# Optimization experiments

Measured on AMD Instinct MI355X. Metric: run time of the kernel, lower is better.

The kernel has to match this reference:

```python
import jax, jax.numpy as jnp
import numpy as np

# ---- static config (from init_kwargs / search_cfg) ----
N, C, CI, H, W_ = 4, 64, 16, 96, 96   # frames, in_ch, inter_ch, height, width
PS, S0, WS, K = 7, 4, 9, 32           # patch size, query stride, search window, top-k
SCALE = 10.0                          # softmax_scale
WH, PP = WS // 2, PS // 2
PAD = WH + PP                         # reflect pad so every candidate patch is valid
nH = H // S0
NQ = nH * nH                          # queries per frame
D = CI * PS * PS                      # patch feature dim


def conv1x1(x, w, b):
    # x: [N,Cin,H,W], w: [Cout,Cin]
    return jnp.einsum('oc,nchw->nohw', w, x) + b[None, :, None, None]


def extract_patches(x):
    # x: [N,CI,H,W] -> [N,Ho,Wo,CI*PS*PS]; patch at index y has center y-WH in image coords
    xp = jnp.pad(x, ((0, 0), (0, 0), (PAD, PAD), (PAD, PAD)), mode='reflect')
    p = jax.lax.conv_general_dilated_patches(xp, (PS, PS), (1, 1), 'VALID')
    return jnp.transpose(p, (0, 2, 3, 1))


def setup_inputs() -> dict:
    key = jax.random.key(0)
    ks = jax.random.split(key, 6)
    s = 0.05
    return {
        'vid': jax.random.normal(ks[0], (N, C, H, W_), jnp.float32),
        'flows': jnp.zeros((N, 2, H, W_), jnp.int32),
        'theta_w': jax.random.normal(ks[1], (CI, C), jnp.float32) * s,
        'theta_b': jnp.zeros((CI,), jnp.float32),
        'phi_w': jax.random.normal(ks[2], (CI, C), jnp.float32) * s,
        'phi_b': jnp.zeros((CI,), jnp.float32),
        'g_w': jax.random.normal(ks[3], (CI, C), jnp.float32) * s,
        'g_b': jnp.zeros((CI,), jnp.float32),
        'w_w': jax.random.normal(ks[4], (C, CI), jnp.float32) * s,
        'w_b': jnp.zeros((C,), jnp.float32),
    }


def reference(vid, flows, theta_w, theta_b, phi_w, phi_b, g_w, g_b, w_w, w_b):
    theta = conv1x1(vid, theta_w, theta_b)   # queries
    phi = conv1x1(vid, phi_w, phi_b)         # keys
    g = conv1x1(vid, g_w, g_b)               # values

    Tp = extract_patches(theta)  # [N,Ho,Wo,D]
    Pp = extract_patches(phi)
    Gp = extract_patches(g)

    # query grid centers (stride0)
    q = jnp.arange(0, H, S0)
    qci = jnp.repeat(q, nH)      # [NQ]
    qcj = jnp.tile(q, nH)

    # flow-guided candidate window (stride1=1, ws x ws offsets)
    off = jnp.arange(WS) - WH
    oi = jnp.repeat(off, WS)     # [WS*WS]
    oj = jnp.tile(off, WS)
    fq = flows[:, :, qci, qcj]   # [N,2,NQ] integer flow at query centers
    ci = jnp.clip(qci[None, :, None] + fq[:, 0, :, None] + oi[None, None, :], 0, H - 1)
    cj = jnp.clip(qcj[None, :, None] + fq[:, 1, :, None] + oj[None, None, :], 0, W_ - 1)
    Yi, Yj = ci + WH, cj + WH    # [N,NQ,WS*WS] indices into patch arrays

    gather = jax.vmap(lambda P, yi, yj: P[yi, yj])

    Qp = Tp[:, qci + WH, qcj + WH, :]            # [N,NQ,D]
    Cg = gather(Pp, Yi, Yj)                      # [N,NQ,WS*WS,D]
    # L2 patch distances
    dist = ((Qp ** 2).sum(-1)[:, :, None] + (Cg ** 2).sum(-1)
            - 2.0 * jnp.einsum('nqd,nqwd->nqw', Qp, Cg))

    negd, idx = jax.lax.top_k(-dist, K)          # k nearest patches
    w = jax.nn.softmax(SCALE * negd, axis=-1)    # softmax(-scale * dist)

    yi_k = jnp.take_along_axis(Yi, idx, axis=2)  # [N,NQ,K]
    yj_k = jnp.take_along_axis(Yj, idx, axis=2)
    Gg = gather(Gp, yi_k, yj_k)                  # [N,NQ,K,D]

    # wpsum: weighted patch sum
    outp = jnp.einsum('nqk,nqkd->nqd', w, Gg).reshape(N, NQ, CI, PS, PS)
    vals = jnp.transpose(outp, (0, 1, 3, 4, 2))  # [N,NQ,PS,PS,CI]

    # fold (overlap-add) back to image, normalized by counts
    ii2 = (qci[:, None] + jnp.arange(PS))[:, :, None]   # [NQ,PS,1] canvas rows
    jj2 = (qcj[:, None] + jnp.arange(PS))[:, None, :]   # [NQ,1,PS] canvas cols
    Hc, Wc = H + 2 * PP, W_ + 2 * PP
    canvas = jnp.zeros((N, Hc, Wc, CI), vid.dtype).at[:, ii2, jj2, :].add(vals)
    cnt = jnp.zeros((Hc, Wc), vid.dtype).at[ii2, jj2].add(jnp.ones((NQ, PS, PS), vid.dtype))
    agg = canvas[:, PP:PP + H, PP:PP + W_] / cnt[PP:PP + H, PP:PP + W_, None]
    agg = jnp.transpose(agg, (0, 3, 1, 2))       # [N,CI,H,W]

    return vid + conv1x1(agg, w_w, w_b)
```

## Files before the change

### kernel.cpp

```cpp
#include <hip/hip_runtime.h>
#include <hip/hip_bf16.h>

#define N_   4
#define C_   64
#define CI_  16
#define H_   96
#define W__  96
#define PS_  7
#define S0_  4
#define WS_  9
#define K_   32
#define WH_  4
#define PP_  3
#define nH_  24
#define NQ_  576
#define D_   784
#define HW_  9216

#define PLS  226
#define QLS  52

__device__ __forceinline__ int rf(int v) {
    v = v < 0 ? -v : v;
    return v > H_ - 1 ? 2 * (H_ - 1) - v : v;
}

__global__ __launch_bounds__(256) void conv_kernel(
    const float* __restrict__ vid,
    const float* __restrict__ tw, const float* __restrict__ tb,
    const float* __restrict__ pw, const float* __restrict__ pb,
    const float* __restrict__ gw, const float* __restrict__ gb,
    float* __restrict__ theta, float* __restrict__ phi, float* __restrict__ g)
{
    int b = blockIdx.x;
    int pbk = b % 144;
    int t2  = b / 144;
    int og  = t2 & 1;
    int arr = t2 >> 1;
    const float* wsel = arr == 0 ? tw : (arr == 1 ? pw : gw);
    const float* bsel = arr == 0 ? tb : (arr == 1 ? pb : gb);
    float*       dsel = arr == 0 ? theta : (arr == 1 ? phi : g);

    int idx = pbk * 256 + threadIdx.x;
    int n = idx / HW_, pix = idx % HW_;
    const float* vp = vid + (size_t)n * C_ * HW_ + pix;
    const float* wp = wsel + og * 8 * C_;

    float acc[8];
#pragma unroll
    for (int o = 0; o < 8; o++) acc[o] = 0.f;

#pragma unroll
    for (int cc = 0; cc < C_; cc += 8) {
        float v[8];
#pragma unroll
        for (int j = 0; j < 8; j++) v[j] = vp[(cc + j) * HW_];
#pragma unroll
        for (int o = 0; o < 8; o++) {
            float4 wa = *(const float4*)&wp[o * C_ + cc];
            float4 wbv = *(const float4*)&wp[o * C_ + cc + 4];
            acc[o] += wa.x * v[0] + wa.y * v[1] + wa.z * v[2] + wa.w * v[3]
                    + wbv.x * v[4] + wbv.y * v[5] + wbv.z * v[6] + wbv.w * v[7];
        }
    }

    size_t ob = (size_t)idx * CI_ + og * 8;
    *(float4*)&dsel[ob + 0] = make_float4(acc[0] + bsel[og * 8 + 0],
                                          acc[1] + bsel[og * 8 + 1],
                                          acc[2] + bsel[og * 8 + 2],
                                          acc[3] + bsel[og * 8 + 3]);
    *(float4*)&dsel[ob + 4] = make_float4(acc[4] + bsel[og * 8 + 4],
                                          acc[5] + bsel[og * 8 + 5],
                                          acc[6] + bsel[og * 8 + 6],
                                          acc[7] + bsel[og * 8 + 7]);
}

__global__ __launch_bounds__(192) void attn_kernel(
    const float* __restrict__ theta, const float* __restrict__ phi,
    const float* __restrict__ g, const int* __restrict__ flows,
    float* __restrict__ outp)
{
    __shared__ float Ql[CI_ * QLS];
    __shared__ float Pl[CI_ * PLS];
    __shared__ float Gl[CI_ * PLS];
    __shared__ float part[81 * 17];
    __shared__ float dist[81];
    __shared__ int   selflag[81];
    __shared__ float wlist[K_];
    __shared__ int   cilist[K_], cjlist[K_];
    __shared__ float dmin_s, esum_s;

    int tid = threadIdx.x;
    int bq  = blockIdx.x;
    int n = bq / NQ_, q0 = bq % NQ_;
    int qi = q0 / nH_, qj = q0 % nH_;
    int qci = qi * S0_, qcj = qj * S0_;

    int f0 = flows[((n * 2 + 0) * H_ + qci) * W__ + qcj];
    int f1 = flows[((n * 2 + 1) * H_ + qci) * W__ + qcj];
    int bi = qci + f0, bj = qcj + f1;
    int loi = min(max(bi - WH_, 0), H_ - 1);
    int loj = min(max(bj - WH_, 0), W__ - 1);

    const float* thn = theta + (size_t)n * HW_ * CI_;
    const float* phn = phi   + (size_t)n * HW_ * CI_;
    const float* gn  = g     + (size_t)n * HW_ * CI_;

    for (int i = tid; i < 49 * 4; i += 192) {
        int px = i >> 2, cg = (i & 3) * 4;
        int r = px / 7, s = px % 7;
        size_t gb = ((size_t)(rf(qci + r - PP_) * W__ + rf(qcj + s - PP_))) * CI_ + cg;
        float4 v = *(const float4*)&thn[gb];
        Ql[(cg + 0) * QLS + px] = v.x;
        Ql[(cg + 1) * QLS + px] = v.y;
        Ql[(cg + 2) * QLS + px] = v.z;
        Ql[(cg + 3) * QLS + px] = v.w;
    }
    for (int i = tid; i < 225 * 4; i += 192) {
        int px = i >> 2, cg = (i & 3) * 4;
        int r = px / 15, s = px % 15;
        size_t gb = ((size_t)(rf(loi + r - PP_) * W__ + rf(loj + s - PP_))) * CI_ + cg;
        float4 pv = *(const float4*)&phn[gb];
        float4 gv = *(const float4*)&gn[gb];
        Pl[(cg + 0) * PLS + px] = pv.x;
        Pl[(cg + 1) * PLS + px] = pv.y;
        Pl[(cg + 2) * PLS + px] = pv.z;
        Pl[(cg + 3) * PLS + px] = pv.w;
        Gl[(cg + 0) * PLS + px] = gv.x;
        Gl[(cg + 1) * PLS + px] = gv.y;
        Gl[(cg + 2) * PLS + px] = gv.z;
        Gl[(cg + 3) * PLS + px] = gv.w;
    }
    if (tid == 0) esum_s = 0.f;
    __syncthreads();

    if (tid < 144) {
        int c  = tid & 15;
        int cj = tid >> 4;
        float qr[49];
#pragma unroll
        for (int i = 0; i < 12; i++) {
            float4 t4 = *(const float4*)&Ql[c * QLS + i * 4];
            qr[i * 4 + 0] = t4.x; qr[i * 4 + 1] = t4.y;
            qr[i * 4 + 2] = t4.z; qr[i * 4 + 3] = t4.w;
        }
        qr[48] = Ql[c * QLS + 48];

        float corr[9], sqv[9];
#pragma unroll
        for (int i = 0; i < 9; i++) { corr[i] = 0.f; sqv[i] = 0.f; }

        const float* Pb = &Pl[c * PLS + cj];
#pragma unroll
        for (int y = 0; y < 15; y++) {
            float seg[7];
#pragma unroll
            for (int s = 0; s < 7; s++) seg[s] = Pb[y * 15 + s];
            float s2 = 0.f;
#pragma unroll
            for (int s = 0; s < 7; s++) s2 += seg[s] * seg[s];
#pragma unroll
            for (int ci = 0; ci < 9; ci++) {
                if (y - ci >= 0 && y - ci < 7) {
                    const int r = y - ci;
                    float t = 0.f;
#pragma unroll
                    for (int s = 0; s < 7; s++) t += qr[r * 7 + s] * seg[s];
                    corr[ci] += t;
                    sqv[ci]  += s2;
                }
            }
        }
#pragma unroll
        for (int ci = 0; ci < 9; ci++)
            part[(cj * 9 + ci) * 17 + c] = sqv[ci] - 2.f * corr[ci];
    }
    __syncthreads();

    if (tid < 81) {
        int wi = tid / WS_, wj = tid % WS_;
        int cil = min(max(bi + wi - WH_, 0), H_ - 1) - loi;
        int cjl = min(max(bj + wj - WH_, 0), W__ - 1) - loj;
        int pidx = cjl * 9 + cil;
        float d = 0.f;
#pragma unroll
        for (int c = 0; c < CI_; c++) d += part[pidx * 17 + c];
        dist[tid] = d;
    }
    __syncthreads();

    if (tid < 81) {
        float d = dist[tid];
        int rank = 0;
        for (int j = 0; j < 81; j++) {
            float dj = dist[j];
            rank += (dj < d) || (dj == d && j < tid);
        }
        selflag[tid] = (rank < K_) ? 1 : 0;
        if (rank == 0) dmin_s = d;
    }
    __syncthreads();

    float e = 0.f;
    int pos = -1;
    if (tid < 81 && selflag[tid]) {
        pos = 0;
        for (int j = 0; j < tid; j++) pos += selflag[j];
        e = expf(10.f * (dmin_s - dist[tid]));
        atomicAdd(&esum_s, e);
    }
    __syncthreads();
    if (pos >= 0) {
        int wi = tid / WS_, wj = tid % WS_;
        wlist[pos]  = e / esum_s;
        cilist[pos] = min(max(bi + wi - WH_, 0), H_ - 1) - loi;
        cjlist[pos] = min(max(bj + wj - WH_, 0), W__ - 1) - loj;
    }
    __syncthreads();

    float wreg[K_];
    int   oreg[K_];
#pragma unroll
    for (int k = 0; k < K_; k++) {
        wreg[k] = wlist[k];
        oreg[k] = cilist[k] * 15 + cjlist[k];
    }
    float* op = outp + (size_t)bq * D_;
    for (int dI = tid; dI < D_; dI += 192) {
        int rs = dI >> 4, c = dI & 15;
        int r = rs / 7, s = rs % 7;
        const float* Gb = &Gl[c * PLS + r * 15 + s];
        float acc = 0.f;
#pragma unroll
        for (int k = 0; k < K_; k++) acc += wreg[k] * Gb[oreg[k]];
        op[dI] = acc;
    }
}

__global__ __launch_bounds__(256) void output_kernel(
    const float* __restrict__ vid, const float* __restrict__ outp,
    const float* __restrict__ ww, const float* __restrict__ wb,
    float* __restrict__ out)
{
    __shared__ float part[32][4][CI_];
    __shared__ float agg_l[32][17];
    __shared__ float w_l[C_ * CI_];
    __shared__ float b_l[C_];

    int tid = threadIdx.x;
    *(float4*)&w_l[tid * 4] = *(const float4*)&ww[tid * 4];
    if (tid < C_) b_l[tid] = wb[tid];

    int gp0 = blockIdx.x * 32;

    if (tid < 128) {
        int px = tid >> 2, cb = tid & 3;
        int idx = gp0 + px;
        int n = idx / HW_, pix = idx % HW_;
        int y = pix / W__, x = pix % W__;
        int thi_i = min(nH_ - 1, (y + PP_) >> 2);
        int thi_j = min(nH_ - 1, (x + PP_) >> 2);
        int qi = (y >> 2) + (cb >> 1);
        int qj = (x >> 2) + (cb & 1);
        float4 r0 = make_float4(0.f, 0.f, 0.f, 0.f), r1 = r0, r2 = r0, r3 = r0;
        if (qi <= thi_i && qj <= thi_j) {
            int a  = y + PP_ - S0_ * qi;
            int bb = x + PP_ - S0_ * qj;
            const float* op = outp +
                (((size_t)n * NQ_ + qi * nH_ + qj) * 49 + a * 7 + bb) * CI_;
            r0 = *(const float4*)&op[0];
            r1 = *(const float4*)&op[4];
            r2 = *(const float4*)&op[8];
            r3 = *(const float4*)&op[12];
        }
        *(float4*)&part[px][cb][0]  = r0;
        *(float4*)&part[px][cb][4]  = r1;
        *(float4*)&part[px][cb][8]  = r2;
        *(float4*)&part[px][cb][12] = r3;
    }
    __syncthreads();

    {
        int px = tid >> 3, c2 = (tid & 7) * 2;
        int idx = gp0 + px;
        int pix = idx % HW_;
        int y = pix / W__, x = pix % W__;
        int ni = min(nH_ - 1, (y + PP_) >> 2) - (y >> 2) + 1;
        int nj = min(nH_ - 1, (x + PP_) >> 2) - (x >> 2) + 1;
        float inv = 1.f / (float)(ni * nj);
#pragma unroll
        for (int k = 0; k < 2; k++) {
            int c = c2 + k;
            agg_l[px][c] = (part[px][0][c] + part[px][1][c] +
                            part[px][2][c] + part[px][3][c]) * inv;
        }
    }
    __syncthreads();

    int og = tid >> 5, px = tid & 31;
    int idx = gp0 + px;
    int n = idx / HW_, pix = idx % HW_;
    float ar[CI_];
#pragma unroll
    for (int c = 0; c < CI_; c++) ar[c] = agg_l[px][c];

    const float* vp  = vid + (size_t)n * C_ * HW_ + pix;
    float*       op2 = out + (size_t)n * C_ * HW_ + pix;
#pragma unroll
    for (int o = 0; o < 8; o++) {
        int co = og * 8 + o;
        float4 w0 = *(const float4*)&w_l[co * CI_ + 0];
        float4 w1 = *(const float4*)&w_l[co * CI_ + 4];
        float4 w2 = *(const float4*)&w_l[co * CI_ + 8];
        float4 w3 = *(const float4*)&w_l[co * CI_ + 12];
        float s = b_l[co];
        s += w0.x * ar[0]  + w0.y * ar[1]  + w0.z * ar[2]  + w0.w * ar[3];
        s += w1.x * ar[4]  + w1.y * ar[5]  + w1.z * ar[6]  + w1.w * ar[7];
        s += w2.x * ar[8]  + w2.y * ar[9]  + w2.z * ar[10] + w2.w * ar[11];
        s += w3.x * ar[12] + w3.y * ar[13] + w3.z * ar[14] + w3.w * ar[15];
        op2[(size_t)co * HW_] = vp[(size_t)co * HW_] + s;
    }
}

extern "C" void kernel_launch(void* const* d_in, const int* in_sizes, int n_in,
                              void* d_out, int out_size, void* d_ws, size_t ws_size,
                              hipStream_t stream) {
    const float* vid   = (const float*)d_in[0];
    const int*   flows = (const int*)  d_in[1];
    const float* tw    = (const float*)d_in[2];
    const float* tb    = (const float*)d_in[3];
    const float* pw    = (const float*)d_in[4];
    const float* pb    = (const float*)d_in[5];
    const float* gw    = (const float*)d_in[6];
    const float* gb    = (const float*)d_in[7];
    const float* ww    = (const float*)d_in[8];
    const float* wb    = (const float*)d_in[9];
    float* out = (float*)d_out;

    float* ws = (float*)d_ws;
    const size_t fsz = (size_t)N_ * HW_ * CI_;
    float* theta = ws;
    float* phi   = ws + fsz;
    float* g     = ws + 2 * fsz;
    float* outp  = ws + 3 * fsz;

    conv_kernel<<<864, 256, 0, stream>>>(
        vid, tw, tb, pw, pb, gw, gb, theta, phi, g);
    attn_kernel<<<N_ * NQ_, 192, 0, stream>>>(theta, phi, g, flows, outp);
    output_kernel<<<1152, 256, 0, stream>>>(vid, outp, ww, wb, out);
}
```

Before: 128.7 us.

## Rework attention block reductions, store values in bf16 LDS, flatten output kernel

The attention kernel moves to 256 threads. It replaces the shared partial-distance buffer with a shuffle reduction across channels, swaps the rank-based selection flags and atomics for a ballot/popcount compaction, and normalises the softmax in registers. The value patch tile is now held in shared memory as bf16 in pixel-major layout, which halves its LDS footprint but lowers precision. The output kernel drops its shared-memory staging and has each thread gather and project its own pixel over a 2D grid, and the conv kernel loads all 64 channels into registers up front.

```diff
diff --git a/kernel.cpp b/kernel.cpp
--- a/kernel.cpp
+++ b/kernel.cpp
@@ -19,6 +19,7 @@
 
 #define PLS  226
 #define QLS  52
+#define GLS  16
 
 __device__ __forceinline__ int rf(int v) {
     v = v < 0 ? -v : v;
@@ -46,21 +47,19 @@
     const float* vp = vid + (size_t)n * C_ * HW_ + pix;
     const float* wp = wsel + og * 8 * C_;
 
+    float v[64];
+#pragma unroll
+    for (int c = 0; c < 64; c++) v[c] = vp[c * HW_];
+
     float acc[8];
 #pragma unroll
     for (int o = 0; o < 8; o++) acc[o] = 0.f;
-
-#pragma unroll
-    for (int cc = 0; cc < C_; cc += 8) {
-        float v[8];
-#pragma unroll
-        for (int j = 0; j < 8; j++) v[j] = vp[(cc + j) * HW_];
-#pragma unroll
-        for (int o = 0; o < 8; o++) {
-            float4 wa = *(const float4*)&wp[o * C_ + cc];
-            float4 wbv = *(const float4*)&wp[o * C_ + cc + 4];
-            acc[o] += wa.x * v[0] + wa.y * v[1] + wa.z * v[2] + wa.w * v[3]
-                    + wbv.x * v[4] + wbv.y * v[5] + wbv.z * v[6] + wbv.w * v[7];
+#pragma unroll
+    for (int o = 0; o < 8; o++) {
+#pragma unroll
+        for (int c = 0; c < 64; c += 4) {
+            float4 w4 = *(const float4*)&wp[o * C_ + c];
+            acc[o] += w4.x * v[c] + w4.y * v[c + 1] + w4.z * v[c + 2] + w4.w * v[c + 3];
         }
     }
 
@@ -75,20 +74,20 @@
                                           acc[7] + bsel[og * 8 + 7]);
 }
 
-__global__ __launch_bounds__(192) void attn_kernel(
+__global__ __launch_bounds__(256) void attn_kernel(
     const float* __restrict__ theta, const float* __restrict__ phi,
     const float* __restrict__ g, const int* __restrict__ flows,
     float* __restrict__ outp)
 {
     __shared__ float Ql[CI_ * QLS];
     __shared__ float Pl[CI_ * PLS];
-    __shared__ float Gl[CI_ * PLS];
-    __shared__ float part[81 * 17];
+    __shared__ __hip_bfloat16 Gl[225 * GLS];
     __shared__ float dist[81];
-    __shared__ int   selflag[81];
+    __shared__ float distW[81];
     __shared__ float wlist[K_];
-    __shared__ int   cilist[K_], cjlist[K_];
-    __shared__ float dmin_s, esum_s;
+    __shared__ int   olist[K_];
+    __shared__ float dmin_s;
+    __shared__ int   cnt0_s;
 
     int tid = threadIdx.x;
     int bq  = blockIdx.x;
@@ -106,8 +105,8 @@
     const float* phn = phi   + (size_t)n * HW_ * CI_;
     const float* gn  = g     + (size_t)n * HW_ * CI_;
 
-    for (int i = tid; i < 49 * 4; i += 192) {
-        int px = i >> 2, cg = (i & 3) * 4;
+    if (tid < 196) {
+        int px = tid >> 2, cg = (tid & 3) * 4;
         int r = px / 7, s = px % 7;
         size_t gb = ((size_t)(rf(qci + r - PP_) * W__ + rf(qcj + s - PP_))) * CI_ + cg;
         float4 v = *(const float4*)&thn[gb];
@@ -116,7 +115,7 @@
         Ql[(cg + 2) * QLS + px] = v.z;
         Ql[(cg + 3) * QLS + px] = v.w;
     }
-    for (int i = tid; i < 225 * 4; i += 192) {
+    for (int i = tid; i < 225 * 4; i += 256) {
         int px = i >> 2, cg = (i & 3) * 4;
         int r = px / 15, s = px % 15;
         size_t gb = ((size_t)(rf(loi + r - PP_) * W__ + rf(loj + s - PP_))) * CI_ + cg;
@@ -126,12 +125,11 @@
         Pl[(cg + 1) * PLS + px] = pv.y;
         Pl[(cg + 2) * PLS + px] = pv.z;
         Pl[(cg + 3) * PLS + px] = pv.w;
-        Gl[(cg + 0) * PLS + px] = gv.x;
-        Gl[(cg + 1) * PLS + px] = gv.y;
-        Gl[(cg + 2) * PLS + px] = gv.z;
-        Gl[(cg + 3) * PLS + px] = gv.w;
-    }
-    if (tid == 0) esum_s = 0.f;
+        Gl[px * GLS + cg + 0] = __float2bfloat16(gv.x);
+        Gl[px * GLS + cg + 1] = __float2bfloat16(gv.y);
+        Gl[px * GLS + cg + 2] = __float2bfloat16(gv.z);
+        Gl[px * GLS + cg + 3] = __float2bfloat16(gv.w);
+    }
     __syncthreads();
 
     if (tid < 144) {
@@ -139,16 +137,16 @@
         int cj = tid >> 4;
         float qr[49];
 #pragma unroll
-        for (int i = 0; i < 12; i++) {
-            float4 t4 = *(const float4*)&Ql[c * QLS + i * 4];
-            qr[i * 4 + 0] = t4.x; qr[i * 4 + 1] = t4.y;
-            qr[i * 4 + 2] = t4.z; qr[i * 4 + 3] = t4.w;
+        for (int i2 = 0; i2 < 12; i2++) {
+            float4 t4 = *(const float4*)&Ql[c * QLS + i2 * 4];
+            qr[i2 * 4 + 0] = t4.x; qr[i2 * 4 + 1] = t4.y;
+            qr[i2 * 4 + 2] = t4.z; qr[i2 * 4 + 3] = t4.w;
         }
         qr[48] = Ql[c * QLS + 48];
 
         float corr[9], sqv[9];
 #pragma unroll
-        for (int i = 0; i < 9; i++) { corr[i] = 0.f; sqv[i] = 0.f; }
+        for (int i2 = 0; i2 < 9; i2++) { corr[i2] = 0.f; sqv[i2] = 0.f; }
 
         const float* Pb = &Pl[c * PLS + cj];
 #pragma unroll
@@ -172,67 +170,71 @@
             }
         }
 #pragma unroll
-        for (int ci = 0; ci < 9; ci++)
-            part[(cj * 9 + ci) * 17 + c] = sqv[ci] - 2.f * corr[ci];
-    }
-    __syncthreads();
-
+        for (int ci = 0; ci < 9; ci++) {
+            float v2 = sqv[ci] - 2.f * corr[ci];
+#pragma unroll
+            for (int m2 = 1; m2 < 16; m2 <<= 1) v2 += __shfl_xor(v2, m2, 16);
+            if (c == ci) dist[cj * 9 + ci] = v2;
+        }
+    }
+    __syncthreads();
+
+    float d = 0.f;
+    int cil = 0, cjl = 0;
     if (tid < 81) {
         int wi = tid / WS_, wj = tid % WS_;
-        int cil = min(max(bi + wi - WH_, 0), H_ - 1) - loi;
-        int cjl = min(max(bj + wj - WH_, 0), W__ - 1) - loj;
-        int pidx = cjl * 9 + cil;
-        float d = 0.f;
-#pragma unroll
-        for (int c = 0; c < CI_; c++) d += part[pidx * 17 + c];
-        dist[tid] = d;
-    }
-    __syncthreads();
-
+        cil = min(max(bi + wi - WH_, 0), H_ - 1) - loi;
+        cjl = min(max(bj + wj - WH_, 0), W__ - 1) - loj;
+        d = dist[cjl * 9 + cil];
+        distW[tid] = d;
+    }
+    __syncthreads();
+
+    bool sel = false;
     if (tid < 81) {
-        float d = dist[tid];
         int rank = 0;
         for (int j = 0; j < 81; j++) {
-            float dj = dist[j];
+            float dj = distW[j];
             rank += (dj < d) || (dj == d && j < tid);
         }
-        selflag[tid] = (rank < K_) ? 1 : 0;
+        sel = rank < K_;
         if (rank == 0) dmin_s = d;
     }
-    __syncthreads();
-
-    float e = 0.f;
-    int pos = -1;
-    if (tid < 81 && selflag[tid]) {
-        pos = 0;
-        for (int j = 0; j < tid; j++) pos += selflag[j];
-        e = expf(10.f * (dmin_s - dist[tid]));
-        atomicAdd(&esum_s, e);
-    }
-    __syncthreads();
-    if (pos >= 0) {
-        int wi = tid / WS_, wj = tid % WS_;
-        wlist[pos]  = e / esum_s;
-        cilist[pos] = min(max(bi + wi - WH_, 0), H_ - 1) - loi;
-        cjlist[pos] = min(max(bj + wj - WH_, 0), W__ - 1) - loj;
+    unsigned long long m = __ballot(sel);
+    if (tid == 0) cnt0_s = __popcll(m);
+    __syncthreads();
+
+    if (sel) {
+        unsigned long long lt = ((unsigned long long)1 << (tid & 63)) - 1;
+        int pos = __popcll(m & lt) + (tid >= 64 ? cnt0_s : 0);
+        float e = expf(10.f * (dmin_s - d));
+        wlist[pos] = e;
+        olist[pos] = cil * 15 + cjl;
     }
     __syncthreads();
 
     float wreg[K_];
     int   oreg[K_];
+    float esum = 0.f;
 #pragma unroll
     for (int k = 0; k < K_; k++) {
         wreg[k] = wlist[k];
-        oreg[k] = cilist[k] * 15 + cjlist[k];
-    }
+        esum += wreg[k];
+        oreg[k] = olist[k] * GLS;
+    }
+    float inv_es = 1.f / esum;
+#pragma unroll
+    for (int k = 0; k < K_; k++) wreg[k] *= inv_es;
+
     float* op = outp + (size_t)bq * D_;
-    for (int dI = tid; dI < D_; dI += 192) {
+    for (int dI = tid; dI < D_; dI += 256) {
         int rs = dI >> 4, c = dI & 15;
         int r = rs / 7, s = rs % 7;
-        const float* Gb = &Gl[c * PLS + r * 15 + s];
+        int base2 = (r * 15 + s) * GLS + c;
         float acc = 0.f;
 #pragma unroll
-        for (int k = 0; k < K_; k++) acc += wreg[k] * Gb[oreg[k]];
+        for (int k = 0; k < K_; k++)
+            acc += wreg[k] * __bfloat162float(Gl[oreg[k] + base2]);
         op[dI] = acc;
     }
 }
@@ -242,82 +244,58 @@
     const float* __restrict__ ww, const float* __restrict__ wb,
     float* __restrict__ out)
 {
-    __shared__ float part[32][4][CI_];
-    __shared__ float agg_l[32][17];
-    __shared__ float w_l[C_ * CI_];
-    __shared__ float b_l[C_];
-
     int tid = threadIdx.x;
-    *(float4*)&w_l[tid * 4] = *(const float4*)&ww[tid * 4];
-    if (tid < C_) b_l[tid] = wb[tid];
-
-    int gp0 = blockIdx.x * 32;
-
-    if (tid < 128) {
-        int px = tid >> 2, cb = tid & 3;
-        int idx = gp0 + px;
-        int n = idx / HW_, pix = idx % HW_;
-        int y = pix / W__, x = pix % W__;
-        int thi_i = min(nH_ - 1, (y + PP_) >> 2);
-        int thi_j = min(nH_ - 1, (x + PP_) >> 2);
-        int qi = (y >> 2) + (cb >> 1);
-        int qj = (x >> 2) + (cb & 1);
-        float4 r0 = make_float4(0.f, 0.f, 0.f, 0.f), r1 = r0, r2 = r0, r3 = r0;
+    int og  = blockIdx.y;
+    int idx = blockIdx.x * 256 + tid;
+    int n = idx / HW_, pix = idx % HW_;
+    int y = pix / W__, x = pix % W__;
+    int tlo_i = y >> 2, tlo_j = x >> 2;
+    int thi_i = min(nH_ - 1, (y + PP_) >> 2);
+    int thi_j = min(nH_ - 1, (x + PP_) >> 2);
+    int ni = thi_i - tlo_i + 1;
+    int nj = thi_j - tlo_j + 1;
+    float inv = 1.f / (float)(ni * nj);
+
+    float agg[CI_];
+#pragma unroll
+    for (int c = 0; c < CI_; c++) agg[c] = 0.f;
+
+#pragma unroll
+    for (int cb = 0; cb < 4; cb++) {
+        int qi = tlo_i + (cb >> 1);
+        int qj = tlo_j + (cb & 1);
         if (qi <= thi_i && qj <= thi_j) {
             int a  = y + PP_ - S0_ * qi;
             int bb = x + PP_ - S0_ * qj;
             const float* op = outp +
                 (((size_t)n * NQ_ + qi * nH_ + qj) * 49 + a * 7 + bb) * CI_;
-            r0 = *(const float4*)&op[0];
-            r1 = *(const float4*)&op[4];
-            r2 = *(const float4*)&op[8];
-            r3 = *(const float4*)&op[12];
-        }
-        *(float4*)&part[px][cb][0]  = r0;
-        *(float4*)&part[px][cb][4]  = r1;
-        *(float4*)&part[px][cb][8]  = r2;
-        *(float4*)&part[px][cb][12] = r3;
-    }
-    __syncthreads();
-
-    {
-        int px = tid >> 3, c2 = (tid & 7) * 2;
-        int idx = gp0 + px;
-        int pix = idx % HW_;
-        int y = pix / W__, x = pix % W__;
-        int ni = min(nH_ - 1, (y + PP_) >> 2) - (y >> 2) + 1;
-        int nj = min(nH_ - 1, (x + PP_) >> 2) - (x >> 2) + 1;
-        float inv = 1.f / (float)(ni * nj);
-#pragma unroll
-        for (int k = 0; k < 2; k++) {
-            int c = c2 + k;
-            agg_l[px][c] = (part[px][0][c] + part[px][1][c] +
-                            part[px][2][c] + part[px][3][c]) * inv;
-        }
-    }
-    __syncthreads();
-
-    int og = tid >> 5, px = tid & 31;
-    int idx = gp0 + px;
-    int n = idx / HW_, pix = idx % HW_;
-    float ar[CI_];
-#pragma unroll
-    for (int c = 0; c < CI_; c++) ar[c] = agg_l[px][c];
+            float4 r0 = *(const float4*)&op[0];
+            float4 r1 = *(const float4*)&op[4];
+            float4 r2 = *(const float4*)&op[8];
+            float4 r3 = *(const float4*)&op[12];
+            agg[0] += r0.x; agg[1] += r0.y; agg[2]  += r0.z; agg[3]  += r0.w;
+            agg[4] += r1.x; agg[5] += r1.y; agg[6]  += r1.z; agg[7]  += r1.w;
+            agg[8] += r2.x; agg[9] += r2.y; agg[10] += r2.z; agg[11] += r2.w;
+            agg[12] += r3.x; agg[13] += r3.y; agg[14] += r3.z; agg[15] += r3.w;
+        }
+    }
+#pragma unroll
+    for (int c = 0; c < CI_; c++) agg[c] *= inv;
 
     const float* vp  = vid + (size_t)n * C_ * HW_ + pix;
     float*       op2 = out + (size_t)n * C_ * HW_ + pix;
 #pragma unroll
-    for (int o = 0; o < 8; o++) {
-        int co = og * 8 + o;
-        float4 w0 = *(const float4*)&w_l[co * CI_ + 0];
-        float4 w1 = *(const float4*)&w_l[co * CI_ + 4];
-        float4 w2 = *(const float4*)&w_l[co * CI_ + 8];
-        float4 w3 = *(const float4*)&w_l[co * CI_ + 12];
-        float s = b_l[co];
-        s += w0.x * ar[0]  + w0.y * ar[1]  + w0.z * ar[2]  + w0.w * ar[3];
-        s += w1.x * ar[4]  + w1.y * ar[5]  + w1.z * ar[6]  + w1.w * ar[7];
-        s += w2.x * ar[8]  + w2.y * ar[9]  + w2.z * ar[10] + w2.w * ar[11];
-        s += w3.x * ar[12] + w3.y * ar[13] + w3.z * ar[14] + w3.w * ar[15];
+    for (int oo = 0; oo < 8; oo++) {
+        int co = og * 8 + oo;
+        float4 w0 = *(const float4*)&ww[co * CI_ + 0];
+        float4 w1 = *(const float4*)&ww[co * CI_ + 4];
+        float4 w2 = *(const float4*)&ww[co * CI_ + 8];
+        float4 w3 = *(const float4*)&ww[co * CI_ + 12];
+        float s = wb[co];
+        s += w0.x * agg[0]  + w0.y * agg[1]  + w0.z * agg[2]  + w0.w * agg[3];
+        s += w1.x * agg[4]  + w1.y * agg[5]  + w1.z * agg[6]  + w1.w * agg[7];
+        s += w2.x * agg[8]  + w2.y * agg[9]  + w2.z * agg[10] + w2.w * agg[11];
+        s += w3.x * agg[12] + w3.y * agg[13] + w3.z * agg[14] + w3.w * agg[15];
         op2[(size_t)co * HW_] = vp[(size_t)co * HW_] + s;
     }
 }
@@ -346,6 +324,6 @@
 
     conv_kernel<<<864, 256, 0, stream>>>(
         vid, tw, tb, pw, pb, gw, gb, theta, phi, g);
-    attn_kernel<<<N_ * NQ_, 192, 0, stream>>>(theta, phi, g, flows, outp);
-    output_kernel<<<1152, 256, 0, stream>>>(vid, outp, ww, wb, out);
-}
+    attn_kernel<<<N_ * NQ_, 256, 0, stream>>>(theta, phi, g, flows, outp);
+    output_kernel<<<dim3(144, 8), 256, 0, stream>>>(vid, outp, ww, wb, out);
+}
```

New measurement: 132.7 us. +3.1%, slower.
